# Performance work log

Hardware: AMD Instinct MI355X
Metric: run time of the kernel (lower is better)

## Reference

```python
import jax, jax.numpy as jnp
import numpy as np
import math

D_K = 64

def setup_inputs() -> dict:
    key = jax.random.key(0)
    kq, kk, kv, km = jax.random.split(key, 4)
    B, H, S, D = 2, 16, 2048, D_K
    Q = jax.random.normal(kq, (B, H, S, D), dtype=jnp.float32)
    K = jax.random.normal(kk, (B, H, S, D), dtype=jnp.float32)
    V = jax.random.normal(kv, (B, H, S, D), dtype=jnp.float32)
    attn_mask = jax.random.randint(km, (B, 1, S, S), 0, 2, dtype=jnp.int32)
    return {"Q": Q, "K": K, "V": V, "attn_mask": attn_mask}

def reference(Q, K, V, attn_mask):
    # scores: [B, H, S, S]
    scores = jnp.einsum('bhqd,bhkd->bhqk', Q, K) / math.sqrt(D_K)
    scores = jnp.where(attn_mask == 0, jnp.float32(-1e9), scores)
    attn = jax.nn.softmax(scores, axis=-1)
    context = jnp.einsum('bhqk,bhkd->bhqd', attn, V)
    return (context, attn)
```

## Files before the change

### kernel.cpp

```cpp
#include <hip/hip_runtime.h>
#include <math.h>

#define B_   2
#define H_   16
#define S_   2048
#define D_   64
#define QT   16
#define NQT  (S_/QT)
#define NBLK (B_*H_*NQT)

typedef __attribute__((ext_vector_type(8))) short  bf16x8;
typedef __attribute__((ext_vector_type(8))) unsigned short u16x8;
typedef __attribute__((ext_vector_type(4))) float  f32x4;

static __device__ __forceinline__ short f2bf(float f) {
    union { float f; unsigned u; } x; x.f = f;
    unsigned r = x.u + 0x7fffu + ((x.u >> 16) & 1u);
    return (short)(r >> 16);
}
static __device__ __forceinline__ float bf2f(unsigned short u) {
    union { unsigned u; float f; } x; x.u = ((unsigned)u) << 16;
    return x.f;
}

__global__ __launch_bounds__(256) void cvtK_kernel(const float* __restrict__ K,
                                                   unsigned short* __restrict__ Kb) {
    const size_t i = ((size_t)blockIdx.x * 256 + threadIdx.x) * 8;
    const float4 a = *(const float4*)(K + i);
    const float4 b = *(const float4*)(K + i + 4);
    u16x8 o;
    o[0]=f2bf(a.x); o[1]=f2bf(a.y); o[2]=f2bf(a.z); o[3]=f2bf(a.w);
    o[4]=f2bf(b.x); o[5]=f2bf(b.y); o[6]=f2bf(b.z); o[7]=f2bf(b.w);
    *(u16x8*)(Kb + i) = o;
}

__global__ __launch_bounds__(256) void cvtVT_kernel(const float* __restrict__ V,
                                                    unsigned short* __restrict__ Vt) {
    const int l  = threadIdx.x & 63;
    const int w  = threadIdx.x >> 6;
    const int bh = blockIdx.x >> 6;
    const int kc = (blockIdx.x & 63) * 32 + w * 8;
    const float* vp = V + ((size_t)bh * S_ + kc) * D_ + l;
    u16x8 o;
    #pragma unroll
    for (int j = 0; j < 8; ++j) o[j] = f2bf(vp[(size_t)j * D_]);
    *(u16x8*)(Vt + ((size_t)bh * D_ + l) * S_ + kc) = o;
}

__global__ __launch_bounds__(256) void maskbits_kernel(const int* __restrict__ M,
                                                       unsigned long long* __restrict__ bits) {
    const int w = threadIdx.x >> 6, l = threadIdx.x & 63;
    const size_t wl0 = (size_t)(blockIdx.x * 4 + w) * 32;
    for (int it = 0; it < 32; ++it) {
        const int mk = M[(wl0 + it) * 64 + l];
        const unsigned long long bm = __ballot(mk != 0);
        if (l == 0) bits[wl0 + it] = bm;
    }
}

template<int PREP>
__global__ __launch_bounds__(256, 2)
void sdpa_mfma_kernel(const float* __restrict__ Q, const float* __restrict__ K,
                      const float* __restrict__ V, const int* __restrict__ M,
                      const unsigned short* __restrict__ Kb,
                      const unsigned short* __restrict__ Vt,
                      const unsigned* __restrict__ bits,
                      float* __restrict__ ctx_out, float* __restrict__ attn_out) {
    __shared__ __align__(16) unsigned short sc[QT][S_];
    __shared__ __align__(16) unsigned mb[QT][64];
    __shared__ float linv[QT];

    const int t  = threadIdx.x;
    const int w  = t >> 6;
    const int l  = t & 63;
    const int lr = l & 15;
    const int lg = l >> 4;

    const int orig = blockIdx.x;
    const int swz  = (orig & 7) * (NBLK / 8) + (orig >> 3);
    const int bh   = swz >> 7;
    const int qt   = swz & 127;
    const int b    = bh >> 4;
    const int q0   = qt * QT;

    const float* Qb = Q + (size_t)bh * S_ * D_;
    const int*   Mb = M + (size_t)b * S_ * S_;

    if (PREP) {
        const int r = t >> 4, cw = (t & 15) * 4;
        *(uint4*)&mb[r][cw] = *(const uint4*)(bits + ((size_t)b * S_ + q0 + r) * 64 + cw);
    }

    bf16x8 aq0, aq1;
    {
        const float* qp = Qb + (size_t)(q0 + lr) * D_ + lg * 8;
        #pragma unroll
        for (int j = 0; j < 8; ++j) aq0[j] = f2bf(0.125f * qp[j]);
        #pragma unroll
        for (int j = 0; j < 8; ++j) aq1[j] = f2bf(0.125f * qp[32 + j]);
    }
    if (PREP) __syncthreads();

    #pragma unroll 2
    for (int kt = 0; kt < 32; ++kt) {
        const int k0 = w * 512 + kt * 16;
        bf16x8 bk0, bk1;
        if (PREP) {
            const unsigned short* kp = Kb + ((size_t)bh * S_ + k0 + lr) * D_ + lg * 8;
            bk0 = *(const bf16x8*)kp;
            bk1 = *(const bf16x8*)(kp + 32);
        } else {
            const float* kp = K + ((size_t)bh * S_ + k0 + lr) * D_ + lg * 8;
            #pragma unroll
            for (int j = 0; j < 8; ++j) bk0[j] = f2bf(kp[j]);
            #pragma unroll
            for (int j = 0; j < 8; ++j) bk1[j] = f2bf(kp[32 + j]);
        }
        f32x4 c = {0.f, 0.f, 0.f, 0.f};
        c = __builtin_amdgcn_mfma_f32_16x16x32_bf16(aq0, bk0, c, 0, 0, 0);
        c = __builtin_amdgcn_mfma_f32_16x16x32_bf16(aq1, bk1, c, 0, 0, 0);
        const int key = k0 + lr;
        #pragma unroll
        for (int r = 0; r < 4; ++r) {
            const int row = lg * 4 + r;
            int mk;
            if (PREP) mk = (mb[row][key >> 5] >> (key & 31)) & 1;
            else      mk = Mb[(size_t)(q0 + row) * S_ + key];
            const float s = mk ? c[r] : -1e9f;
            sc[row][(((key >> 3) ^ (row & 7)) << 3) + (key & 7)] = (unsigned short)f2bf(s);
        }
    }
    __syncthreads();

    #pragma unroll
    for (int r = 0; r < 4; ++r) {
        const int q = w * 4 + r;
        const int x = q & 7;
        float f[32];
        #pragma unroll
        for (int i = 0; i < 4; ++i) {
            const u16x8 u = *(const u16x8*)&sc[q][(i * 64 + l) * 8];
            #pragma unroll
            for (int j = 0; j < 8; ++j) f[i * 8 + j] = bf2f(u[j]);
        }
        float m = f[0];
        #pragma unroll
        for (int j = 1; j < 32; ++j) m = fmaxf(m, f[j]);
        #pragma unroll
        for (int off = 32; off; off >>= 1) m = fmaxf(m, __shfl_xor(m, off));
        float ssum = 0.f;
        #pragma unroll
        for (int j = 0; j < 32; ++j) { f[j] = __expf(f[j] - m); ssum += f[j]; }
        #pragma unroll
        for (int off = 32; off; off >>= 1) ssum += __shfl_xor(ssum, off);
        const float il = 1.0f / ssum;
        if (l == 0) linv[q] = il;

        float* arow = attn_out + ((size_t)bh * S_ + q0 + q) * S_;
        #pragma unroll
        for (int i = 0; i < 4; ++i) {
            const int us = i * 64 + l;
            u16x8 ub;
            #pragma unroll
            for (int j = 0; j < 8; ++j) ub[j] = (unsigned short)f2bf(f[i * 8 + j]);
            *(u16x8*)&sc[q][us * 8] = ub;
            const int uk = us ^ x;
            float4 o0, o1;
            o0.x = f[i*8+0]*il; o0.y = f[i*8+1]*il; o0.z = f[i*8+2]*il; o0.w = f[i*8+3]*il;
            o1.x = f[i*8+4]*il; o1.y = f[i*8+5]*il; o1.z = f[i*8+6]*il; o1.w = f[i*8+7]*il;
            *(float4*)(arow + (size_t)uk * 8)     = o0;
            *(float4*)(arow + (size_t)uk * 8 + 4) = o1;
        }
    }
    __syncthreads();

    {
        const int d0 = w * 16;
        f32x4 cc = {0.f, 0.f, 0.f, 0.f};
        #pragma unroll 2
        for (int ks = 0; ks < 64; ++ks) {
            const int k0 = ks * 32;
            const int un = ((k0 >> 3) + lg) ^ (lr & 7);
            const bf16x8 pa = *(const bf16x8*)&sc[lr][un * 8];
            bf16x8 vb;
            if (PREP) {
                vb = *(const bf16x8*)(Vt + ((size_t)bh * D_ + d0 + lr) * S_ + k0 + lg * 8);
            } else {
                const float* vp = V + ((size_t)bh * S_ + k0 + lg * 8) * D_ + d0 + lr;
                #pragma unroll
                for (int j = 0; j < 8; ++j) vb[j] = f2bf(vp[(size_t)j * D_]);
            }
            cc = __builtin_amdgcn_mfma_f32_16x16x32_bf16(pa, vb, cc, 0, 0, 0);
        }
        #pragma unroll
        for (int r = 0; r < 4; ++r) {
            const int q = lg * 4 + r;
            ctx_out[((size_t)bh * S_ + q0 + q) * D_ + d0 + lr] = cc[r] * linv[q];
        }
    }
}

extern "C" void kernel_launch(void* const* d_in, const int* in_sizes, int n_in,
                              void* d_out, int out_size, void* d_ws, size_t ws_size,
                              hipStream_t stream) {
    const float* Q = (const float*)d_in[0];
    const float* K = (const float*)d_in[1];
    const float* V = (const float*)d_in[2];
    const int*   M = (const int*)d_in[3];

    float* ctx  = (float*)d_out;
    float* attn = (float*)d_out + (size_t)B_ * H_ * S_ * D_;

    const size_t nEl      = (size_t)B_ * H_ * S_ * D_;
    const size_t nBits64  = (size_t)B_ * S_ * (S_ / 64);
    const size_t need     = nEl * 2 * 2 + nBits64 * 8;

    if (ws_size >= need) {
        unsigned short* Kb = (unsigned short*)d_ws;
        unsigned short* Vt = Kb + nEl;
        unsigned long long* bits = (unsigned long long*)(Vt + nEl);
        cvtK_kernel    <<<dim3((int)(nEl / 2048)), dim3(256), 0, stream>>>(K, Kb);
        cvtVT_kernel   <<<dim3(B_ * H_ * (S_ / 32)), dim3(256), 0, stream>>>(V, Vt);
        maskbits_kernel<<<dim3((int)(nBits64 / 128)), dim3(256), 0, stream>>>(M, bits);
        sdpa_mfma_kernel<1><<<dim3(NBLK), dim3(256), 0, stream>>>(
            Q, K, V, M, Kb, Vt, (const unsigned*)bits, ctx, attn);
    } else {
        sdpa_mfma_kernel<0><<<dim3(NBLK), dim3(256), 0, stream>>>(
            Q, K, V, M, nullptr, nullptr, nullptr, ctx, attn);
    }
}
```

Baseline: 374.9 us.

## Replace LDS score buffer with two-pass online-softmax recompute and register P·V

The attention kernel no longer stores the full 16x2048 bf16 score row block in LDS. A first pass computes QK^T and keeps online max and sum statistics per row. A second pass recomputes QK^T, writes the normalized attention probabilities, and feeds the bf16-packed probabilities to the PV MFMA through cross-lane shuffles, with partial context summed across waves in LDS. Less LDS per block lets the launch bound rise to 4 blocks per CU, and Q is pre-converted to bf16 in a separate kernel. The cost is doubled QK^T work and K reads, plus extra exp evaluations.

```diff
diff --git a/kernel.cpp b/kernel.cpp
--- a/kernel.cpp
+++ b/kernel.cpp
@@ -18,20 +18,22 @@
     unsigned r = x.u + 0x7fffu + ((x.u >> 16) & 1u);
     return (short)(r >> 16);
 }
-static __device__ __forceinline__ float bf2f(unsigned short u) {
-    union { unsigned u; float f; } x; x.u = ((unsigned)u) << 16;
-    return x.f;
-}
-
-__global__ __launch_bounds__(256) void cvtK_kernel(const float* __restrict__ K,
-                                                   unsigned short* __restrict__ Kb) {
+static __device__ __forceinline__ unsigned pk_bf16(float lo, float hi) {
+    unsigned r;
+    asm("v_cvt_pk_bf16_f32 %0, %1, %2" : "=v"(r) : "v"(lo), "v"(hi));
+    return r;
+}
+
+__global__ __launch_bounds__(256) void cvt_scale_kernel(const float* __restrict__ src,
+                                                        unsigned short* __restrict__ dst,
+                                                        float scale) {
     const size_t i = ((size_t)blockIdx.x * 256 + threadIdx.x) * 8;
-    const float4 a = *(const float4*)(K + i);
-    const float4 b = *(const float4*)(K + i + 4);
+    const float4 a = *(const float4*)(src + i);
+    const float4 b = *(const float4*)(src + i + 4);
     u16x8 o;
-    o[0]=f2bf(a.x); o[1]=f2bf(a.y); o[2]=f2bf(a.z); o[3]=f2bf(a.w);
-    o[4]=f2bf(b.x); o[5]=f2bf(b.y); o[6]=f2bf(b.z); o[7]=f2bf(b.w);
-    *(u16x8*)(Kb + i) = o;
+    o[0]=f2bf(a.x*scale); o[1]=f2bf(a.y*scale); o[2]=f2bf(a.z*scale); o[3]=f2bf(a.w*scale);
+    o[4]=f2bf(b.x*scale); o[5]=f2bf(b.y*scale); o[6]=f2bf(b.z*scale); o[7]=f2bf(b.w*scale);
+    *(u16x8*)(dst + i) = o;
 }
 
 __global__ __launch_bounds__(256) void cvtVT_kernel(const float* __restrict__ V,
@@ -59,22 +61,23 @@
 }
 
 template<int PREP>
-__global__ __launch_bounds__(256, 2)
-void sdpa_mfma_kernel(const float* __restrict__ Q, const float* __restrict__ K,
-                      const float* __restrict__ V, const int* __restrict__ M,
-                      const unsigned short* __restrict__ Kb,
-                      const unsigned short* __restrict__ Vt,
-                      const unsigned* __restrict__ bits,
-                      float* __restrict__ ctx_out, float* __restrict__ attn_out) {
-    __shared__ __align__(16) unsigned short sc[QT][S_];
-    __shared__ __align__(16) unsigned mb[QT][64];
-    __shared__ float linv[QT];
-
-    const int t  = threadIdx.x;
-    const int w  = t >> 6;
-    const int l  = t & 63;
-    const int lr = l & 15;
-    const int lg = l >> 4;
+__global__ __launch_bounds__(256, 4)
+void sdpa_2pass_kernel(const float* __restrict__ Qf, const float* __restrict__ Kf,
+                       const float* __restrict__ Vf, const int* __restrict__ Mi,
+                       const unsigned short* __restrict__ Qs,
+                       const unsigned short* __restrict__ Kb,
+                       const unsigned short* __restrict__ Vt,
+                       const unsigned* __restrict__ bits,
+                       float* __restrict__ ctx_out, float* __restrict__ attn_out) {
+    __shared__ unsigned mb[QT][66];
+    __shared__ float red[4][QT][2];
+    __shared__ float ctxp[4][QT][68];
+
+    const int t = threadIdx.x;
+    const int w = t >> 6;
+    const int l = t & 63;
+    const int x = l & 15;
+    const int g = l >> 4;
 
     const int orig = blockIdx.x;
     const int swz  = (orig & 7) * (NBLK / 8) + (orig >> 3);
@@ -83,120 +86,148 @@
     const int b    = bh >> 4;
     const int q0   = qt * QT;
 
-    const float* Qb = Q + (size_t)bh * S_ * D_;
-    const int*   Mb = M + (size_t)b * S_ * S_;
-
     if (PREP) {
-        const int r = t >> 4, cw = (t & 15) * 4;
-        *(uint4*)&mb[r][cw] = *(const uint4*)(bits + ((size_t)b * S_ + q0 + r) * 64 + cw);
-    }
-
-    bf16x8 aq0, aq1;
-    {
-        const float* qp = Qb + (size_t)(q0 + lr) * D_ + lg * 8;
-        #pragma unroll
-        for (int j = 0; j < 8; ++j) aq0[j] = f2bf(0.125f * qp[j]);
-        #pragma unroll
-        for (int j = 0; j < 8; ++j) aq1[j] = f2bf(0.125f * qp[32 + j]);
+        #pragma unroll
+        for (int i = 0; i < 4; ++i) {
+            const int flat = t * 4 + i;
+            mb[flat >> 6][flat & 63] =
+                bits[((size_t)b * S_ + q0 + (flat >> 6)) * 64 + (flat & 63)];
+        }
+    }
+
+    bf16x8 bq0, bq1;
+    if (PREP) {
+        const unsigned short* qp = Qs + ((size_t)bh * S_ + q0 + x) * D_ + g * 8;
+        bq0 = *(const bf16x8*)qp;
+        bq1 = *(const bf16x8*)(qp + 32);
+    } else {
+        const float* qp = Qf + ((size_t)bh * S_ + q0 + x) * D_ + g * 8;
+        #pragma unroll
+        for (int j = 0; j < 8; ++j) bq0[j] = f2bf(0.125f * qp[j]);
+        #pragma unroll
+        for (int j = 0; j < 8; ++j) bq1[j] = f2bf(0.125f * qp[32 + j]);
     }
     if (PREP) __syncthreads();
 
-    #pragma unroll 2
+    auto qk_tile = [&](int ktg, f32x4& c) {
+        bf16x8 ak0, ak1;
+        if (PREP) {
+            const unsigned short* kp = Kb + ((size_t)bh * S_ + ktg * 16 + x) * D_ + g * 8;
+            ak0 = *(const bf16x8*)kp;
+            ak1 = *(const bf16x8*)(kp + 32);
+        } else {
+            const float* kp = Kf + ((size_t)bh * S_ + ktg * 16 + x) * D_ + g * 8;
+            #pragma unroll
+            for (int j = 0; j < 8; ++j) ak0[j] = f2bf(kp[j]);
+            #pragma unroll
+            for (int j = 0; j < 8; ++j) ak1[j] = f2bf(kp[32 + j]);
+        }
+        c[0]=0.f; c[1]=0.f; c[2]=0.f; c[3]=0.f;
+        c = __builtin_amdgcn_mfma_f32_16x16x32_bf16(ak0, bq0, c, 0, 0, 0);
+        c = __builtin_amdgcn_mfma_f32_16x16x32_bf16(ak1, bq1, c, 0, 0, 0);
+        if (PREP) {
+            const unsigned word = mb[x][ktg >> 1];
+            const int base = 16 * (ktg & 1) + 4 * g;
+            #pragma unroll
+            for (int r = 0; r < 4; ++r)
+                if (!((word >> (base + r)) & 1u)) c[r] = -1e9f;
+        } else {
+            const int* mp = Mi + ((size_t)b * S_ + q0 + x) * S_ + ktg * 16 + 4 * g;
+            #pragma unroll
+            for (int r = 0; r < 4; ++r)
+                if (!mp[r]) c[r] = -1e9f;
+        }
+    };
+
+    float m = -INFINITY, ssum = 0.f;
     for (int kt = 0; kt < 32; ++kt) {
-        const int k0 = w * 512 + kt * 16;
-        bf16x8 bk0, bk1;
-        if (PREP) {
-            const unsigned short* kp = Kb + ((size_t)bh * S_ + k0 + lr) * D_ + lg * 8;
-            bk0 = *(const bf16x8*)kp;
-            bk1 = *(const bf16x8*)(kp + 32);
-        } else {
-            const float* kp = K + ((size_t)bh * S_ + k0 + lr) * D_ + lg * 8;
-            #pragma unroll
-            for (int j = 0; j < 8; ++j) bk0[j] = f2bf(kp[j]);
-            #pragma unroll
-            for (int j = 0; j < 8; ++j) bk1[j] = f2bf(kp[32 + j]);
-        }
-        f32x4 c = {0.f, 0.f, 0.f, 0.f};
-        c = __builtin_amdgcn_mfma_f32_16x16x32_bf16(aq0, bk0, c, 0, 0, 0);
-        c = __builtin_amdgcn_mfma_f32_16x16x32_bf16(aq1, bk1, c, 0, 0, 0);
-        const int key = k0 + lr;
-        #pragma unroll
-        for (int r = 0; r < 4; ++r) {
-            const int row = lg * 4 + r;
-            int mk;
-            if (PREP) mk = (mb[row][key >> 5] >> (key & 31)) & 1;
-            else      mk = Mb[(size_t)(q0 + row) * S_ + key];
-            const float s = mk ? c[r] : -1e9f;
-            sc[row][(((key >> 3) ^ (row & 7)) << 3) + (key & 7)] = (unsigned short)f2bf(s);
-        }
-    }
+        f32x4 c; qk_tile(32 * w + kt, c);
+        const float tm = fmaxf(fmaxf(c[0], c[1]), fmaxf(c[2], c[3]));
+        const float nm = fmaxf(m, tm);
+        ssum = ssum * __expf(m - nm)
+             + __expf(c[0] - nm) + __expf(c[1] - nm)
+             + __expf(c[2] - nm) + __expf(c[3] - nm);
+        m = nm;
+    }
+    #pragma unroll
+    for (int off = 16; off <= 32; off <<= 1) {
+        const float mo = __shfl_xor(m, off), so = __shfl_xor(ssum, off);
+        const float nm = fmaxf(m, mo);
+        ssum = ssum * __expf(m - nm) + so * __expf(mo - nm);
+        m = nm;
+    }
+    if (l < 16) { red[w][l][0] = m; red[w][l][1] = ssum; }
     __syncthreads();
-
-    #pragma unroll
-    for (int r = 0; r < 4; ++r) {
-        const int q = w * 4 + r;
-        const int x = q & 7;
-        float f[32];
-        #pragma unroll
-        for (int i = 0; i < 4; ++i) {
-            const u16x8 u = *(const u16x8*)&sc[q][(i * 64 + l) * 8];
-            #pragma unroll
-            for (int j = 0; j < 8; ++j) f[i * 8 + j] = bf2f(u[j]);
-        }
-        float m = f[0];
-        #pragma unroll
-        for (int j = 1; j < 32; ++j) m = fmaxf(m, f[j]);
-        #pragma unroll
-        for (int off = 32; off; off >>= 1) m = fmaxf(m, __shfl_xor(m, off));
-        float ssum = 0.f;
-        #pragma unroll
-        for (int j = 0; j < 32; ++j) { f[j] = __expf(f[j] - m); ssum += f[j]; }
-        #pragma unroll
-        for (int off = 32; off; off >>= 1) ssum += __shfl_xor(ssum, off);
-        const float il = 1.0f / ssum;
-        if (l == 0) linv[q] = il;
-
-        float* arow = attn_out + ((size_t)bh * S_ + q0 + q) * S_;
-        #pragma unroll
-        for (int i = 0; i < 4; ++i) {
-            const int us = i * 64 + l;
-            u16x8 ub;
-            #pragma unroll
-            for (int j = 0; j < 8; ++j) ub[j] = (unsigned short)f2bf(f[i * 8 + j]);
-            *(u16x8*)&sc[q][us * 8] = ub;
-            const int uk = us ^ x;
-            float4 o0, o1;
-            o0.x = f[i*8+0]*il; o0.y = f[i*8+1]*il; o0.z = f[i*8+2]*il; o0.w = f[i*8+3]*il;
-            o1.x = f[i*8+4]*il; o1.y = f[i*8+5]*il; o1.z = f[i*8+6]*il; o1.w = f[i*8+7]*il;
-            *(float4*)(arow + (size_t)uk * 8)     = o0;
-            *(float4*)(arow + (size_t)uk * 8 + 4) = o1;
-        }
-    }
-    __syncthreads();
-
-    {
-        const int d0 = w * 16;
-        f32x4 cc = {0.f, 0.f, 0.f, 0.f};
-        #pragma unroll 2
-        for (int ks = 0; ks < 64; ++ks) {
-            const int k0 = ks * 32;
-            const int un = ((k0 >> 3) + lg) ^ (lr & 7);
-            const bf16x8 pa = *(const bf16x8*)&sc[lr][un * 8];
+    float M = -INFINITY, S = 0.f;
+    #pragma unroll
+    for (int wv = 0; wv < 4; ++wv) {
+        const float mo = red[wv][x][0], so = red[wv][x][1];
+        const float nm = fmaxf(M, mo);
+        S = S * __expf(M - nm) + so * __expf(mo - nm);
+        M = nm;
+    }
+    const float il = 1.0f / S;
+
+    f32x4 ctx[4];
+    #pragma unroll
+    for (int ds = 0; ds < 4; ++ds) { ctx[ds][0]=0.f; ctx[ds][1]=0.f; ctx[ds][2]=0.f; ctx[ds][3]=0.f; }
+
+    const int laneA = x + 32 * (g & 1);
+    const int laneB = laneA + 16;
+    const int tsel  = g >> 1;
+
+    for (int s = 0; s < 16; ++s) {
+        unsigned W00, W01, W10, W11;
+        #pragma unroll
+        for (int u = 0; u < 2; ++u) {
+            const int ktg = 32 * w + 2 * s + u;
+            f32x4 c; qk_tile(ktg, c);
+            const float p0 = __expf(c[0] - M) * il, p1 = __expf(c[1] - M) * il;
+            const float p2 = __expf(c[2] - M) * il, p3 = __expf(c[3] - M) * il;
+            float4 o; o.x = p0; o.y = p1; o.z = p2; o.w = p3;
+            *(float4*)(attn_out + ((size_t)bh * S_ + q0 + x) * S_ + ktg * 16 + 4 * g) = o;
+            const unsigned lo = pk_bf16(p0, p1), hi = pk_bf16(p2, p3);
+            if (u == 0) { W00 = lo; W01 = hi; } else { W10 = lo; W11 = hi; }
+        }
+        const unsigned a00 = __shfl(W00, laneA), a10 = __shfl(W10, laneA);
+        const unsigned a01 = __shfl(W01, laneA), a11 = __shfl(W11, laneA);
+        const unsigned b00 = __shfl(W00, laneB), b10 = __shfl(W10, laneB);
+        const unsigned b01 = __shfl(W01, laneB), b11 = __shfl(W11, laneB);
+        union { unsigned u[4]; bf16x8 v; } pa;
+        pa.u[0] = tsel ? a10 : a00;
+        pa.u[1] = tsel ? a11 : a01;
+        pa.u[2] = tsel ? b10 : b00;
+        pa.u[3] = tsel ? b11 : b01;
+        const int kb = 512 * w + 32 * s;
+        #pragma unroll
+        for (int ds = 0; ds < 4; ++ds) {
             bf16x8 vb;
             if (PREP) {
-                vb = *(const bf16x8*)(Vt + ((size_t)bh * D_ + d0 + lr) * S_ + k0 + lg * 8);
+                vb = *(const bf16x8*)(Vt + ((size_t)bh * D_ + 16 * ds + x) * S_ + kb + 8 * g);
             } else {
-                const float* vp = V + ((size_t)bh * S_ + k0 + lg * 8) * D_ + d0 + lr;
+                const float* vp = Vf + ((size_t)bh * S_ + kb + 8 * g) * D_ + 16 * ds + x;
                 #pragma unroll
                 for (int j = 0; j < 8; ++j) vb[j] = f2bf(vp[(size_t)j * D_]);
             }
-            cc = __builtin_amdgcn_mfma_f32_16x16x32_bf16(pa, vb, cc, 0, 0, 0);
-        }
-        #pragma unroll
-        for (int r = 0; r < 4; ++r) {
-            const int q = lg * 4 + r;
-            ctx_out[((size_t)bh * S_ + q0 + q) * D_ + d0 + lr] = cc[r] * linv[q];
-        }
+            ctx[ds] = __builtin_amdgcn_mfma_f32_16x16x32_bf16(pa.v, vb, ctx[ds], 0, 0, 0);
+        }
+    }
+
+    #pragma unroll
+    for (int ds = 0; ds < 4; ++ds)
+        #pragma unroll
+        for (int r = 0; r < 4; ++r)
+            ctxp[w][4 * g + r][16 * ds + x] = ctx[ds][r];
+    __syncthreads();
+    {
+        const int base = t * 4;
+        const int qr = base >> 6, c0 = base & 63;
+        float4 o;
+        o.x = ctxp[0][qr][c0+0] + ctxp[1][qr][c0+0] + ctxp[2][qr][c0+0] + ctxp[3][qr][c0+0];
+        o.y = ctxp[0][qr][c0+1] + ctxp[1][qr][c0+1] + ctxp[2][qr][c0+1] + ctxp[3][qr][c0+1];
+        o.z = ctxp[0][qr][c0+2] + ctxp[1][qr][c0+2] + ctxp[2][qr][c0+2] + ctxp[3][qr][c0+2];
+        o.w = ctxp[0][qr][c0+3] + ctxp[1][qr][c0+3] + ctxp[2][qr][c0+3] + ctxp[3][qr][c0+3];
+        *(float4*)(ctx_out + ((size_t)bh * S_ + q0 + qr) * D_ + c0) = o;
     }
 }
 
@@ -211,21 +242,23 @@
     float* ctx  = (float*)d_out;
     float* attn = (float*)d_out + (size_t)B_ * H_ * S_ * D_;
 
-    const size_t nEl      = (size_t)B_ * H_ * S_ * D_;
-    const size_t nBits64  = (size_t)B_ * S_ * (S_ / 64);
-    const size_t need     = nEl * 2 * 2 + nBits64 * 8;
+    const size_t nEl     = (size_t)B_ * H_ * S_ * D_;
+    const size_t nBits64 = (size_t)B_ * S_ * (S_ / 64);
+    const size_t need    = nEl * 2 * 3 + nBits64 * 8;
 
     if (ws_size >= need) {
-        unsigned short* Kb = (unsigned short*)d_ws;
+        unsigned short* Qs = (unsigned short*)d_ws;
+        unsigned short* Kb = Qs + nEl;
         unsigned short* Vt = Kb + nEl;
         unsigned long long* bits = (unsigned long long*)(Vt + nEl);
-        cvtK_kernel    <<<dim3((int)(nEl / 2048)), dim3(256), 0, stream>>>(K, Kb);
-        cvtVT_kernel   <<<dim3(B_ * H_ * (S_ / 32)), dim3(256), 0, stream>>>(V, Vt);
-        maskbits_kernel<<<dim3((int)(nBits64 / 128)), dim3(256), 0, stream>>>(M, bits);
-        sdpa_mfma_kernel<1><<<dim3(NBLK), dim3(256), 0, stream>>>(
-            Q, K, V, M, Kb, Vt, (const unsigned*)bits, ctx, attn);
+        cvt_scale_kernel<<<dim3((int)(nEl / 2048)), dim3(256), 0, stream>>>(Q, Qs, 0.125f);
+        cvt_scale_kernel<<<dim3((int)(nEl / 2048)), dim3(256), 0, stream>>>(K, Kb, 1.0f);
+        cvtVT_kernel    <<<dim3(B_ * H_ * (S_ / 32)), dim3(256), 0, stream>>>(V, Vt);
+        maskbits_kernel <<<dim3((int)(nBits64 / 128)), dim3(256), 0, stream>>>(M, bits);
+        sdpa_2pass_kernel<1><<<dim3(NBLK), dim3(256), 0, stream>>>(
+            Q, K, V, M, Qs, Kb, Vt, (const unsigned*)bits, ctx, attn);
     } else {
-        sdpa_mfma_kernel<0><<<dim3(NBLK), dim3(256), 0, stream>>>(
-            Q, K, V, M, nullptr, nullptr, nullptr, ctx, attn);
-    }
-}
+        sdpa_2pass_kernel<0><<<dim3(NBLK), dim3(256), 0, stream>>>(
+            Q, K, V, M, nullptr, nullptr, nullptr, nullptr, ctx, attn);
+    }
+}
```

After: 426.6 us. 13.8% more time.
